# Optimization experiments

Hardware: AMD Instinct MI355X
Metric: run time of the kernel (lower is better)

The kernel has to match this reference:

```python
import jax, jax.numpy as jnp
import numpy as np

B, T, C = 4, 2048, 2048
H, D = 16, 128  # n_heads, head_dim


def _rope_freqs(seq_len, head_dim, base=10000.0):
    half = head_dim // 2
    inv = 1.0 / (base ** (np.arange(half, dtype=np.float32) / half))
    t = np.arange(seq_len, dtype=np.float32)
    ang = np.outer(t, inv)  # (T, D/2)
    return jnp.asarray(np.stack([np.cos(ang), np.sin(ang)], axis=-1))  # (T, D/2, 2)


def setup_inputs() -> dict:
    key = jax.random.key(0)
    k1, k2, k3 = jax.random.split(key, 3)
    x = jax.random.normal(k1, (B, T, C), dtype=jnp.float32)
    freqs = _rope_freqs(T, D)
    # additive causal mask
    mask = jnp.where(jnp.tril(jnp.ones((T, T), dtype=bool)), 0.0, -1e9).astype(jnp.float32)
    w_qkv = jax.random.normal(k2, (3 * C, C), dtype=jnp.float32) * (1.0 / np.sqrt(C))
    w_out = jax.random.normal(k3, (C, C), dtype=jnp.float32) * (1.0 / np.sqrt(C))
    return {"x": x, "freqs": freqs, "mask": mask, "w_qkv": w_qkv, "w_out": w_out}


def apply_rope(x, freqs):
    # x: (B,H,T,D), freqs: (T,D/2,2)
    xr = x.reshape(*x.shape[:-1], -1, 2)
    cos, sin = freqs[..., 0], freqs[..., 1]
    x0, x1 = xr[..., 0], xr[..., 1]
    rot = jnp.stack([x0 * cos - x1 * sin, x0 * sin + x1 * cos], axis=-1)
    return rot.reshape(x.shape)


def reference(x, freqs, mask, w_qkv, w_out):
    b, t, c = x.shape
    qkv = jnp.einsum('btc,fc->btf', x, w_qkv).reshape(b, t, 3, H, D)
    q, k, v = jnp.moveaxis(qkv, 2, 0)          # each (b,t,H,D)
    q = jnp.transpose(q, (0, 2, 1, 3))          # (b,H,t,D)
    k = jnp.transpose(k, (0, 2, 1, 3))
    v = jnp.transpose(v, (0, 2, 1, 3))
    q = apply_rope(q, freqs[:t])
    k = apply_rope(k, freqs[:t])
    scale = 1.0 / np.sqrt(D).astype(np.float32)
    attn = jnp.einsum('bhqd,bhkd->bhqk', q, k) * scale + mask[:t, :t]
    attn = jax.nn.softmax(attn, axis=-1)
    out = jnp.einsum('bhqk,bhkd->bhqd', attn, v)
    out = jnp.transpose(out, (0, 2, 1, 3)).reshape(b, t, c)
    return jnp.einsum('btc,fc->btf', out, w_out)
```

## Files before the change

kernel.cpp:

```cpp
#include <hip/hip_runtime.h>

typedef unsigned short u16;
typedef unsigned int   u32;

using sx8   = __attribute__((ext_vector_type(8))) short;
using f32x4 = __attribute__((ext_vector_type(4))) float;
using u16x8 = __attribute__((ext_vector_type(8))) unsigned short;

#define BB 4
#define TT 2048
#define CC 2048
#define HH 16
#define DD 128
#define FF 6144
#define MM 8192

static __device__ __forceinline__ u16 f2bf(float f) {
    u32 u = __builtin_bit_cast(u32, f);
    u32 lsb = (u >> 16) & 1u;
    u += 0x7fffu + lsb;
    return (u16)(u >> 16);
}
static __device__ __forceinline__ float bf2f(u16 b) {
    return __builtin_bit_cast(float, (u32)b << 16);
}
static __device__ __forceinline__ f32x4 mfma16(sx8 a, sx8 b, f32x4 c) {
    return __builtin_amdgcn_mfma_f32_16x16x32_bf16(a, b, c, 0, 0, 0);
}
static __device__ __forceinline__ u32 pkbf(float a, float b) {
    return (u32)f2bf(a) | ((u32)f2bf(b) << 16);
}

__global__ __launch_bounds__(256) void k_cvt(const float* __restrict__ src,
                                             u16* __restrict__ dst, int n8) {
    int i = blockIdx.x * 256 + threadIdx.x;
    if (i >= n8) return;
    const float4* s = (const float4*)src;
    float4 a = s[2 * (size_t)i], b = s[2 * (size_t)i + 1];
    u16x8 r;
    r[0] = f2bf(a.x); r[1] = f2bf(a.y); r[2] = f2bf(a.z); r[3] = f2bf(a.w);
    r[4] = f2bf(b.x); r[5] = f2bf(b.y); r[6] = f2bf(b.z); r[7] = f2bf(b.w);
    *(u16x8*)(dst + 8 * (size_t)i) = r;
}

template <int OUTF32>
__global__ __launch_bounds__(512, 2) void k_gemm(const u16* __restrict__ A,
                                                 const u16* __restrict__ Bt,
                                                 float* __restrict__ Cf,
                                                 u16* __restrict__ Cb,
                                                 int M, int N, int K) {
    __shared__ __align__(16) u16 sA[4][256 * 32];
    __shared__ __align__(16) u16 sB[4][256 * 32];
    const int nbm = M >> 8;
    const int rpx = nbm >> 3;
    const int fid = blockIdx.x;
    const int xcd = fid & 7, idx = fid >> 3;
    const int m0 = (xcd * rpx + (idx % rpx)) << 8;
    const int n0 = (idx / rpx) << 8;

    const int tid = threadIdx.x, w = tid >> 6, l = tid & 63;
    const int wm = w >> 2, wn = w & 3;
    const int lr = l & 15, lg = l >> 4;
    const int nk = K >> 5;

    const int srow = tid >> 2;
    const int sg   = tid & 3;
    const int ssg  = sg ^ ((srow >> 1) & 3);
    const u16* pA0 = A  + (size_t)(m0 + srow)       * K + ssg * 8;
    const u16* pA1 = A  + (size_t)(m0 + srow + 128) * K + ssg * 8;
    const u16* pB0 = Bt + (size_t)(n0 + srow)       * K + ssg * 8;
    const u16* pB1 = Bt + (size_t)(n0 + srow + 128) * K + ssg * 8;
    const int dst0 = w * 512;

    const int gA = lg ^ ((lr >> 1) & 3);
    const int raOff = (wm * 128 + lr) * 32 + gA * 8;
    const int rbOff = (wn * 64 + lr) * 32 + gA * 8;

    f32x4 acc[8][4] = {};

#define GLL(SRC, DST) __builtin_amdgcn_global_load_lds( \
        (const __attribute__((address_space(1))) void*)(SRC), \
        (__attribute__((address_space(3))) void*)(DST), 16, 0, 0)

#pragma unroll
    for (int kt = 0; kt < 3; ++kt) {
        GLL(pA0 + kt * 32, &sA[kt][dst0]);
        GLL(pA1 + kt * 32, &sA[kt][4096 + dst0]);
        GLL(pB0 + kt * 32, &sB[kt][dst0]);
        GLL(pB1 + kt * 32, &sB[kt][4096 + dst0]);
    }

#pragma unroll 1
    for (int kt = 0; kt < nk; ++kt) {
        asm volatile("s_waitcnt lgkmcnt(0)" ::: "memory");
        if (kt + 2 < nk)      asm volatile("s_waitcnt vmcnt(8)" ::: "memory");
        else if (kt + 1 < nk) asm volatile("s_waitcnt vmcnt(4)" ::: "memory");
        else                  asm volatile("s_waitcnt vmcnt(0)" ::: "memory");
        __builtin_amdgcn_sched_barrier(0);
        __builtin_amdgcn_s_barrier();
        __builtin_amdgcn_sched_barrier(0);
        const u16* bufA = sA[kt & 3];
        const u16* bufB = sB[kt & 3];
        const bool stg = (kt + 3) < nk;
        const int bw = (kt + 3) & 3;
        if (stg) {
            GLL(pA0 + (kt + 3) * 32, &sA[bw][dst0]);
            GLL(pA1 + (kt + 3) * 32, &sA[bw][4096 + dst0]);
        }
        sx8 af[4], bf[4];
#pragma unroll
        for (int mi = 0; mi < 4; ++mi) af[mi] = *(const sx8*)(bufA + raOff + mi * 512);
#pragma unroll
        for (int ni = 0; ni < 4; ++ni) bf[ni] = *(const sx8*)(bufB + rbOff + ni * 512);
        __builtin_amdgcn_s_setprio(1);
#pragma unroll
        for (int mi = 0; mi < 4; ++mi)
#pragma unroll
            for (int ni = 0; ni < 4; ++ni)
                acc[mi][ni] = mfma16(af[mi], bf[ni], acc[mi][ni]);
        __builtin_amdgcn_s_setprio(0);
        __builtin_amdgcn_s_barrier();
        __builtin_amdgcn_sched_barrier(0);
        if (stg) {
            GLL(pB0 + (kt + 3) * 32, &sB[bw][dst0]);
            GLL(pB1 + (kt + 3) * 32, &sB[bw][4096 + dst0]);
        }
        sx8 ag[4];
#pragma unroll
        for (int mi = 0; mi < 4; ++mi) ag[mi] = *(const sx8*)(bufA + raOff + (mi + 4) * 512);
        __builtin_amdgcn_s_setprio(1);
#pragma unroll
        for (int mi = 0; mi < 4; ++mi)
#pragma unroll
            for (int ni = 0; ni < 4; ++ni)
                acc[mi + 4][ni] = mfma16(ag[mi], bf[ni], acc[mi + 4][ni]);
        __builtin_amdgcn_s_setprio(0);
    }
#undef GLL

#pragma unroll
    for (int mi = 0; mi < 8; ++mi) {
        const int mr = m0 + wm * 128 + mi * 16 + lg * 4;
#pragma unroll
        for (int ni = 0; ni < 4; ++ni) {
            const int nc = n0 + wn * 64 + ni * 16 + lr;
#pragma unroll
            for (int rg = 0; rg < 4; ++rg) {
                float v = acc[mi][ni][rg];
                size_t off = (size_t)(mr + rg) * N + nc;
                if (OUTF32) Cf[off] = v;
                else        Cb[off] = f2bf(v);
            }
        }
    }
}

__global__ __launch_bounds__(256) void k_rope(const u16* __restrict__ qkv,
                                              const float* __restrict__ freqs,
                                              u16* __restrict__ Qo,
                                              u16* __restrict__ Ko,
                                              u16* __restrict__ Vt) {
    const int t0 = blockIdx.x * 64, h = blockIdx.y, b = blockIdx.z;
    const int tid = threadIdx.x;
    const float scale = 0.08838834764831845f;
    __shared__ u16 vt[64][129];
#pragma unroll
    for (int it = 0; it < 16; ++it) {
        int idx = tid + it * 256;
        int trow = idx >> 6, pr = idx & 63;
        int t = t0 + trow;
        size_t ib = (size_t)(b * TT + t) * FF + h * DD + 2 * pr;
        float2 cs = *(const float2*)(freqs + (size_t)t * DD + 2 * pr);
        size_t ob = ((size_t)(b * HH + h) * TT + t) * DD + 2 * pr;
        {
            u32 qp = *(const u32*)(qkv + ib);
            float x0 = bf2f((u16)(qp & 0xffff)), x1 = bf2f((u16)(qp >> 16));
            u32 r = (u32)f2bf((x0 * cs.x - x1 * cs.y) * scale) |
                    ((u32)f2bf((x0 * cs.y + x1 * cs.x) * scale) << 16);
            *(u32*)(Qo + ob) = r;
        }
        {
            u32 kp = *(const u32*)(qkv + ib + CC);
            float x0 = bf2f((u16)(kp & 0xffff)), x1 = bf2f((u16)(kp >> 16));
            u32 r = (u32)f2bf(x0 * cs.x - x1 * cs.y) |
                    ((u32)f2bf(x0 * cs.y + x1 * cs.x) << 16);
            *(u32*)(Ko + ob) = r;
        }
        {
            u32 vp = *(const u32*)(qkv + ib + 2 * CC);
            vt[trow][2 * pr]     = (u16)(vp & 0xffff);
            vt[trow][2 * pr + 1] = (u16)(vp >> 16);
        }
    }
    __syncthreads();
    const size_t vb = (size_t)(b * HH + h) * DD * TT + t0;
#pragma unroll
    for (int it = 0; it < 32; ++it) {
        int idx = tid + it * 256;
        int d = idx >> 6, tr = idx & 63;
        Vt[vb + (size_t)d * TT + tr] = vt[tr][d];
    }
}

#define KV 64
#define PST 68

__global__ __launch_bounds__(256, 2) void k_attn(const u16* __restrict__ Q,
                                                 const u16* __restrict__ K,
                                                 const u16* __restrict__ Vt,
                                                 u16* __restrict__ AO) {
    const int fid = blockIdx.x + 8 * blockIdx.y + 128 * blockIdx.z;
    const int xg = fid >> 6;
    const int hb = fid & 63;
    const int h = hb & 15, b = hb >> 4;

    const int tid = threadIdx.x, w = tid >> 6, l = tid & 63;
    const int lr = l & 15, lg = l >> 4;
    const size_t bh = (size_t)(b * HH + h);
    const u16* Qh = Q + bh * TT * DD;
    const u16* Kh = K + bh * TT * DD;
    const u16* Vh = Vt + bh * DD * TT;

    __shared__ __align__(16) u16 sK[2][KV * DD];
    __shared__ __align__(16) u16 sP[4][32 * PST];
    u16* myP = sP[w];

    const int strow = tid >> 4;
    const int sc16  = tid & 15;

    for (int rep = 0; rep < 2; ++rep) {
        const int g = rep ? (15 - xg) : xg;
        const int q0w = g * 128 + w * 32;
        const int nt = 2 * g + 2;

        sx8 qf[2][4];
#pragma unroll
        for (int i = 0; i < 2; i++)
#pragma unroll
            for (int kk = 0; kk < 4; kk++)
                qf[i][kk] = *(const sx8*)(Qh + (size_t)(q0w + i * 16 + lr) * DD + kk * 32 + lg * 8);

        f32x4 o[2][8] = {};
        float mrow[2] = {-1e30f, -1e30f};
        float lrow[2] = {0.0f, 0.0f};

#pragma unroll
        for (int i = 0; i < 4; ++i) {
            const int row = i * 16 + strow;
            const int scol = (sc16 ^ (row & 7)) * 8;
            __builtin_amdgcn_global_load_lds(
                (const __attribute__((address_space(1))) void*)(Kh + (size_t)row * DD + scol),
                (__attribute__((address_space(3))) void*)(&sK[0][i * 2048 + w * 512]),
                16, 0, 0);
        }
        __syncthreads();

        int cur = 0;
        for (int t = 0; t < nt; ++t) {
            const int k0 = t * KV;
            if (t + 1 < nt) {
                const int kn = k0 + KV;
#pragma unroll
                for (int i = 0; i < 4; ++i) {
                    const int row = i * 16 + strow;
                    const int scol = (sc16 ^ (row & 7)) * 8;
                    __builtin_amdgcn_global_load_lds(
                        (const __attribute__((address_space(1))) void*)(Kh + (size_t)(kn + row) * DD + scol),
                        (__attribute__((address_space(3))) void*)(&sK[cur ^ 1][i * 2048 + w * 512]),
                        16, 0, 0);
                }
            }
            if (k0 <= q0w) {
                f32x4 st[2][4] = {};
#pragma unroll
                for (int j = 0; j < 4; ++j) {
                    const int row = j * 16 + lr;
                    const int rx = row & 7;
                    sx8 kf[4];
#pragma unroll
                    for (int kk = 0; kk < 4; ++kk) {
                        const int c16 = (kk * 4 + lg) ^ rx;
                        kf[kk] = *(const sx8*)(&sK[cur][row * DD + c16 * 8]);
                    }
#pragma unroll
                    for (int kk = 0; kk < 4; ++kk) {
                        st[0][j] = mfma16(kf[kk], qf[0][kk], st[0][j]);
                        st[1][j] = mfma16(kf[kk], qf[1][kk], st[1][j]);
                    }
                }
                sx8 vf0[8];
#pragma unroll
                for (int n = 0; n < 8; ++n)
                    vf0[n] = *(const sx8*)(Vh + (size_t)(n * 16 + lr) * TT + k0 + lg * 8);

                const bool need_mask = (k0 + 63 > q0w);
                const int klocal = lg * 4;
#pragma unroll
                for (int i = 0; i < 2; ++i) {
                    if (need_mask) {
                        const int cl = q0w + i * 16 + lr - k0;
#pragma unroll
                        for (int j = 0; j < 4; ++j)
#pragma unroll
                            for (int rg = 0; rg < 4; ++rg)
                                if (j * 16 + klocal + rg > cl) st[i][j][rg] = -1e30f;
                    }
                    f32x4 m4;
#pragma unroll
                    for (int rg = 0; rg < 4; ++rg)
                        m4[rg] = fmaxf(fmaxf(st[i][0][rg], st[i][1][rg]),
                                       fmaxf(st[i][2][rg], st[i][3][rg]));
                    float pm = fmaxf(fmaxf(m4[0], m4[1]), fmaxf(m4[2], m4[3]));
                    pm = fmaxf(pm, __shfl_xor(pm, 16));
                    pm = fmaxf(pm, __shfl_xor(pm, 32));
                    const float mold = mrow[i];
                    const bool resc = pm > mold + 8.0f;
                    const float mnew = resc ? pm : mold;
                    mrow[i] = mnew;
                    float rs = 0.0f;
#pragma unroll
                    for (int j = 0; j < 4; ++j) {
                        float p0 = __expf(st[i][j][0] - mnew);
                        float p1 = __expf(st[i][j][1] - mnew);
                        float p2 = __expf(st[i][j][2] - mnew);
                        float p3 = __expf(st[i][j][3] - mnew);
                        rs += (p0 + p1) + (p2 + p3);
                        *(uint2*)(myP + (i * 16 + lr) * PST + j * 16 + klocal) =
                            make_uint2(pkbf(p0, p1), pkbf(p2, p3));
                    }
                    rs += __shfl_xor(rs, 16);
                    rs += __shfl_xor(rs, 32);
                    const float sf = resc ? __expf(mold - mnew) : 1.0f;
                    lrow[i] = lrow[i] * sf + rs;
                    if (__any(resc)) {
                        f32x4 sfo;
#pragma unroll
                        for (int rg = 0; rg < 4; ++rg)
                            sfo[rg] = __shfl(sf, 4 * lg + rg);
#pragma unroll
                        for (int n = 0; n < 8; ++n) o[i][n] *= sfo;
                    }
                }
                asm volatile("s_waitcnt lgkmcnt(0)" ::: "memory");
                __builtin_amdgcn_sched_barrier(0);

                sx8 pa0[2], pa1[2];
                pa0[0] = *(const sx8*)(myP + (size_t)lr * PST + lg * 8);
                pa0[1] = *(const sx8*)(myP + (size_t)(16 + lr) * PST + lg * 8);
                pa1[0] = *(const sx8*)(myP + (size_t)lr * PST + 32 + lg * 8);
                pa1[1] = *(const sx8*)(myP + (size_t)(16 + lr) * PST + 32 + lg * 8);
#pragma unroll
                for (int n = 0; n < 8; ++n) {
                    o[0][n] = mfma16(pa0[0], vf0[n], o[0][n]);
                    o[1][n] = mfma16(pa0[1], vf0[n], o[1][n]);
                }
#pragma unroll
                for (int n = 0; n < 8; ++n) {
                    sx8 vf1 = *(const sx8*)(Vh + (size_t)(n * 16 + lr) * TT + k0 + 32 + lg * 8);
                    o[0][n] = mfma16(pa1[0], vf1, o[0][n]);
                    o[1][n] = mfma16(pa1[1], vf1, o[1][n]);
                }
            }
            __syncthreads();
            cur ^= 1;
        }

#pragma unroll
        for (int i = 0; i < 2; ++i) {
            f32x4 linv;
#pragma unroll
            for (int rg = 0; rg < 4; ++rg)
                linv[rg] = __shfl(lrow[i], 4 * lg + rg);
#pragma unroll
            for (int rg = 0; rg < 4; ++rg) {
                const float inv = 1.0f / linv[rg];
                const int tq = q0w + i * 16 + lg * 4 + rg;
                u16* orow = AO + ((size_t)(b * TT) + tq) * CC + h * DD + lr;
#pragma unroll
                for (int n = 0; n < 8; ++n)
                    orow[n * 16] = f2bf(o[i][n][rg] * inv);
            }
        }
    }
}

extern "C" void kernel_launch(void* const* d_in, const int* in_sizes, int n_in,
                              void* d_out, int out_size, void* d_ws, size_t ws_size,
                              hipStream_t stream) {
    const float* x     = (const float*)d_in[0];
    const float* freqs = (const float*)d_in[1];
    const float* w_qkv = (const float*)d_in[3];
    const float* w_out = (const float*)d_in[4];
    float* out = (float*)d_out;

    u16* ws   = (u16*)d_ws;
    u16* xb   = ws;
    u16* wqb  = xb   + (size_t)MM * CC;
    u16* wob  = wqb  + (size_t)FF * CC;
    u16* qkvb = wob  + (size_t)CC * CC;
    u16* Qr   = qkvb + (size_t)MM * FF;
    u16* Kr   = Qr   + (size_t)MM * CC;
    u16* Vt   = Kr   + (size_t)MM * CC;
    u16* AO   = qkvb;

    k_cvt<<<MM * CC / 2048, 256, 0, stream>>>(x, xb, MM * CC / 8);
    k_cvt<<<FF * CC / 2048, 256, 0, stream>>>(w_qkv, wqb, FF * CC / 8);
    k_cvt<<<CC * CC / 2048, 256, 0, stream>>>(w_out, wob, CC * CC / 8);

    k_gemm<0><<<(MM / 256) * (FF / 256), 512, 0, stream>>>(xb, wqb, nullptr, qkvb, MM, FF, CC);
    k_rope<<<dim3(TT / 64, HH, BB), 256, 0, stream>>>(qkvb, freqs, Qr, Kr, Vt);
    k_attn<<<dim3(8, HH, BB), 256, 0, stream>>>(Qr, Kr, Vt, AO);
    k_gemm<1><<<(MM / 256) * (CC / 256), 512, 0, stream>>>(AO, wob, out, nullptr, MM, CC, CC);
}
```

Baseline: 537.3 us.

## Restructure GEMM mainloop to 64-wide K tiles with double-buffered interleaved staging

The bf16 GEMM mainloop now uses 64-element K tiles held in two LDS buffers instead of 32-element tiles in a four-deep ring. Each iteration is split into four MFMA phases, and the global-to-LDS loads for A (next tile) and B (two tiles ahead) are interleaved between those phases. The LDS layout gets a new 8-way XOR swizzle. The intent is to halve the loop and barrier overhead per unit of K and to hide load latency inside the compute phases, at the cost of more barriers per iteration and fragile wait-count bookkeeping.

```diff
diff --git a/kernel.cpp b/kernel.cpp
--- a/kernel.cpp
+++ b/kernel.cpp
@@ -49,8 +49,8 @@
                                                  float* __restrict__ Cf,
                                                  u16* __restrict__ Cb,
                                                  int M, int N, int K) {
-    __shared__ __align__(16) u16 sA[4][256 * 32];
-    __shared__ __align__(16) u16 sB[4][256 * 32];
+    __shared__ __align__(16) u16 sA[2][16384];
+    __shared__ __align__(16) u16 sB[2][16384];
     const int nbm = M >> 8;
     const int rpx = nbm >> 3;
     const int fid = blockIdx.x;
@@ -61,81 +61,107 @@
     const int tid = threadIdx.x, w = tid >> 6, l = tid & 63;
     const int wm = w >> 2, wn = w & 3;
     const int lr = l & 15, lg = l >> 4;
-    const int nk = K >> 5;
-
-    const int srow = tid >> 2;
-    const int sg   = tid & 3;
-    const int ssg  = sg ^ ((srow >> 1) & 3);
-    const u16* pA0 = A  + (size_t)(m0 + srow)       * K + ssg * 8;
-    const u16* pA1 = A  + (size_t)(m0 + srow + 128) * K + ssg * 8;
-    const u16* pB0 = Bt + (size_t)(n0 + srow)       * K + ssg * 8;
-    const u16* pB1 = Bt + (size_t)(n0 + srow + 128) * K + ssg * 8;
-    const int dst0 = w * 512;
-
-    const int gA = lg ^ ((lr >> 1) & 3);
-    const int raOff = (wm * 128 + lr) * 32 + gA * 8;
-    const int rbOff = (wn * 64 + lr) * 32 + gA * 8;
-
-    f32x4 acc[8][4] = {};
+    const int nk = K >> 6;
+
+    const int sg = (l & 7) ^ (l >> 3);
+    const u16* gA = A  + (size_t)(m0 + w * 16 + (l >> 3)) * K + sg * 8;
+    const u16* gB = Bt + (size_t)(n0 + w * 16 + (l >> 3)) * K + sg * 8;
+    const size_t rowK8 = (size_t)8 * K;
+    const size_t halfK = (size_t)128 * K;
 
 #define GLL(SRC, DST) __builtin_amdgcn_global_load_lds( \
         (const __attribute__((address_space(1))) void*)(SRC), \
         (__attribute__((address_space(3))) void*)(DST), 16, 0, 0)
-
-#pragma unroll
-    for (int kt = 0; kt < 3; ++kt) {
-        GLL(pA0 + kt * 32, &sA[kt][dst0]);
-        GLL(pA1 + kt * 32, &sA[kt][4096 + dst0]);
-        GLL(pB0 + kt * 32, &sB[kt][dst0]);
-        GLL(pB1 + kt * 32, &sB[kt][4096 + dst0]);
+#define STAGE_A(tt, hf) do { \
+        const u16* _s = gA + (size_t)(hf) * halfK + (size_t)(tt) * 64; \
+        u16* _d = &sA[(tt) & 1][(hf) * 8192 + w * 1024]; \
+        GLL(_s, _d); GLL(_s + rowK8, _d + 512); } while (0)
+#define STAGE_B(tt, hf) do { \
+        const u16* _s = gB + (size_t)(hf) * halfK + (size_t)(tt) * 64; \
+        u16* _d = &sB[(tt) & 1][(hf) * 8192 + w * 1024]; \
+        GLL(_s, _d); GLL(_s + rowK8, _d + 512); } while (0)
+
+    const int rx = lr & 7;
+    const int rsw0 = ((0 + lg) ^ rx) * 8;
+    const int rsw1 = ((4 + lg) ^ rx) * 8;
+    const int aoff0 = wm * 8192 + lr * 64 + rsw0;
+    const int aoff1 = wm * 8192 + lr * 64 + rsw1;
+    const int boff0 = (wn >> 1) * 8192 + ((wn & 1) * 64 + lr) * 64 + rsw0;
+    const int boff1 = (wn >> 1) * 8192 + ((wn & 1) * 64 + lr) * 64 + rsw1;
+
+    f32x4 acc[8][4] = {};
+
+    STAGE_B(0, 0); STAGE_B(0, 1); STAGE_A(0, 0); STAGE_A(0, 1);
+    STAGE_B(1, 0); STAGE_B(1, 1);
+    asm volatile("s_waitcnt vmcnt(4)" ::: "memory");
+    __builtin_amdgcn_s_barrier();
+
+#pragma unroll 1
+    for (int t = 0; t < nk; ++t) {
+        const u16* bA = sA[t & 1];
+        const u16* bB = sB[t & 1];
+        sx8 a0[8], a1[8], b0[4], b1[4];
+        if (t + 1 < nk) STAGE_A(t + 1, 0);
+#pragma unroll
+        for (int mi = 0; mi < 8; ++mi) a0[mi] = *(const sx8*)(bA + aoff0 + mi * 1024);
+#pragma unroll
+        for (int ni = 0; ni < 4; ++ni) b0[ni] = *(const sx8*)(bB + boff0 + ni * 1024);
+        __builtin_amdgcn_s_barrier();
+        asm volatile("s_waitcnt lgkmcnt(0)" ::: "memory");
+        __builtin_amdgcn_sched_barrier(0);
+        __builtin_amdgcn_s_setprio(1);
+#pragma unroll
+        for (int mi = 0; mi < 8; ++mi) {
+            acc[mi][0] = mfma16(a0[mi], b0[0], acc[mi][0]);
+            acc[mi][1] = mfma16(a0[mi], b0[1], acc[mi][1]);
+        }
+        __builtin_amdgcn_s_setprio(0);
+        __builtin_amdgcn_s_barrier();
+        if (t + 1 < nk) STAGE_A(t + 1, 1);
+#pragma unroll
+        for (int ni = 0; ni < 4; ++ni) b1[ni] = *(const sx8*)(bB + boff1 + ni * 1024);
+        __builtin_amdgcn_s_barrier();
+        asm volatile("s_waitcnt lgkmcnt(0)" ::: "memory");
+        __builtin_amdgcn_sched_barrier(0);
+        __builtin_amdgcn_s_setprio(1);
+#pragma unroll
+        for (int mi = 0; mi < 8; ++mi) {
+            acc[mi][2] = mfma16(a0[mi], b0[2], acc[mi][2]);
+            acc[mi][3] = mfma16(a0[mi], b0[3], acc[mi][3]);
+        }
+        __builtin_amdgcn_s_setprio(0);
+        __builtin_amdgcn_s_barrier();
+        if (t + 2 < nk) STAGE_B(t + 2, 0);
+#pragma unroll
+        for (int mi = 0; mi < 8; ++mi) a1[mi] = *(const sx8*)(bA + aoff1 + mi * 1024);
+        __builtin_amdgcn_s_barrier();
+        asm volatile("s_waitcnt lgkmcnt(0)" ::: "memory");
+        __builtin_amdgcn_sched_barrier(0);
+        __builtin_amdgcn_s_setprio(1);
+#pragma unroll
+        for (int mi = 0; mi < 8; ++mi) {
+            acc[mi][0] = mfma16(a1[mi], b1[0], acc[mi][0]);
+            acc[mi][1] = mfma16(a1[mi], b1[1], acc[mi][1]);
+        }
+        __builtin_amdgcn_s_setprio(0);
+        __builtin_amdgcn_s_barrier();
+        if (t + 2 < nk) STAGE_B(t + 2, 1);
+        __builtin_amdgcn_s_barrier();
+        asm volatile("s_waitcnt lgkmcnt(0)" ::: "memory");
+        __builtin_amdgcn_sched_barrier(0);
+        __builtin_amdgcn_s_setprio(1);
+#pragma unroll
+        for (int mi = 0; mi < 8; ++mi) {
+            acc[mi][2] = mfma16(a1[mi], b1[2], acc[mi][2]);
+            acc[mi][3] = mfma16(a1[mi], b1[3], acc[mi][3]);
+        }
+        __builtin_amdgcn_s_setprio(0);
+        if (t + 2 < nk) asm volatile("s_waitcnt vmcnt(4)" ::: "memory");
+        else            asm volatile("s_waitcnt vmcnt(0)" ::: "memory");
+        __builtin_amdgcn_s_barrier();
     }
-
-#pragma unroll 1
-    for (int kt = 0; kt < nk; ++kt) {
-        asm volatile("s_waitcnt lgkmcnt(0)" ::: "memory");
-        if (kt + 2 < nk)      asm volatile("s_waitcnt vmcnt(8)" ::: "memory");
-        else if (kt + 1 < nk) asm volatile("s_waitcnt vmcnt(4)" ::: "memory");
-        else                  asm volatile("s_waitcnt vmcnt(0)" ::: "memory");
-        __builtin_amdgcn_sched_barrier(0);
-        __builtin_amdgcn_s_barrier();
-        __builtin_amdgcn_sched_barrier(0);
-        const u16* bufA = sA[kt & 3];
-        const u16* bufB = sB[kt & 3];
-        const bool stg = (kt + 3) < nk;
-        const int bw = (kt + 3) & 3;
-        if (stg) {
-            GLL(pA0 + (kt + 3) * 32, &sA[bw][dst0]);
-            GLL(pA1 + (kt + 3) * 32, &sA[bw][4096 + dst0]);
-        }
-        sx8 af[4], bf[4];
-#pragma unroll
-        for (int mi = 0; mi < 4; ++mi) af[mi] = *(const sx8*)(bufA + raOff + mi * 512);
-#pragma unroll
-        for (int ni = 0; ni < 4; ++ni) bf[ni] = *(const sx8*)(bufB + rbOff + ni * 512);
-        __builtin_amdgcn_s_setprio(1);
-#pragma unroll
-        for (int mi = 0; mi < 4; ++mi)
-#pragma unroll
-            for (int ni = 0; ni < 4; ++ni)
-                acc[mi][ni] = mfma16(af[mi], bf[ni], acc[mi][ni]);
-        __builtin_amdgcn_s_setprio(0);
-        __builtin_amdgcn_s_barrier();
-        __builtin_amdgcn_sched_barrier(0);
-        if (stg) {
-            GLL(pB0 + (kt + 3) * 32, &sB[bw][dst0]);
-            GLL(pB1 + (kt + 3) * 32, &sB[bw][4096 + dst0]);
-        }
-        sx8 ag[4];
-#pragma unroll
-        for (int mi = 0; mi < 4; ++mi) ag[mi] = *(const sx8*)(bufA + raOff + (mi + 4) * 512);
-        __builtin_amdgcn_s_setprio(1);
-#pragma unroll
-        for (int mi = 0; mi < 4; ++mi)
-#pragma unroll
-            for (int ni = 0; ni < 4; ++ni)
-                acc[mi + 4][ni] = mfma16(ag[mi], bf[ni], acc[mi + 4][ni]);
-        __builtin_amdgcn_s_setprio(0);
-    }
+#undef STAGE_A
+#undef STAGE_B
 #undef GLL
 
 #pragma unroll
```

Result: no change. 547.7 us (+1.9%).
